# Kernel optimization log

Hardware: AMD Instinct MI355X
Metric: run time of the kernel (lower is better)

## Reference

```python
import jax, jax.numpy as jnp
import numpy as np

HIDDEN = 32
DN = ('NCHW', 'OIHW', 'NCHW')


def setup_inputs() -> dict:
    key = jax.random.key(0)
    ks = jax.random.split(key, 16)
    B = 32768
    s = lambda *sh: 1.0 / np.sqrt(np.prod(sh[1:]) if len(sh) > 1 else sh[0])
    inp = {
        'x': jax.random.normal(ks[0], (B, 12, 3, 4, 4), jnp.float32),
        'hour': jax.random.uniform(ks[1], (B, 1), jnp.float32),
        # ConvLSTM cell: Conv2d(3+32 -> 4*32, k=3, pad=1)
        'conv_w': jax.random.normal(ks[2], (4 * HIDDEN, 3 + HIDDEN, 3, 3), jnp.float32) * 0.05,
        'conv_b': jnp.zeros((4 * HIDDEN,), jnp.float32),
        # hour embedding: Linear(1,16) -> ReLU -> Linear(16,32)
        'he_w1': jax.random.normal(ks[3], (1, 16), jnp.float32),
        'he_b1': jnp.zeros((16,), jnp.float32),
        'he_w2': jax.random.normal(ks[4], (16, 32), jnp.float32) * 0.25,
        'he_b2': jnp.zeros((32,), jnp.float32),
        # decoder: Linear(544,256) -> ReLU -> Linear(256,128) -> ReLU -> Linear(128,30) -> Sigmoid
        'd_w1': jax.random.normal(ks[5], (32 * 4 * 4 + 32, 256), jnp.float32) * 0.04,
        'd_b1': jnp.zeros((256,), jnp.float32),
        'd_w2': jax.random.normal(ks[6], (256, 128), jnp.float32) * 0.06,
        'd_b2': jnp.zeros((128,), jnp.float32),
        'd_w3': jax.random.normal(ks[7], (128, 30), jnp.float32) * 0.09,
        'd_b3': jnp.zeros((30,), jnp.float32),
    }
    return inp


def _convlstm_scan(x, conv_w, conv_b):
    B, T, C, H, W = x.shape
    h0 = jnp.zeros((B, HIDDEN, H, W), x.dtype)
    c0 = jnp.zeros((B, HIDDEN, H, W), x.dtype)

    def step(carry, xt):
        h, c = carry
        inp = jnp.concatenate([xt, h], axis=1)  # [B, 3+32, 4, 4]
        gates = jax.lax.conv_general_dilated(
            inp, conv_w, (1, 1), 'SAME', dimension_numbers=DN)
        gates = gates + conv_b[None, :, None, None]
        i, f, o, g = jnp.split(gates, 4, axis=1)
        c_next = jax.nn.sigmoid(f) * c + jax.nn.sigmoid(i) * jnp.tanh(g)
        h_next = jax.nn.sigmoid(o) * jnp.tanh(c_next)
        return (h_next, c_next), None

    xs = jnp.swapaxes(x, 0, 1)  # [T, B, C, H, W]
    (h, c), _ = jax.lax.scan(step, (h0, c0), xs)
    return h


def reference(x, hour, conv_w, conv_b, he_w1, he_b1, he_w2, he_b2,
              d_w1, d_b1, d_w2, d_b2, d_w3, d_b3):
    B = x.shape[0]
    h = _convlstm_scan(x, conv_w, conv_b)            # [B, 32, 4, 4]
    spatial = h.reshape(B, -1)                        # [B, 512]
    hf = jax.nn.relu(hour @ he_w1 + he_b1) @ he_w2 + he_b2  # [B, 32]
    z = jnp.concatenate([spatial, hf], axis=1)        # [B, 544]
    z = jax.nn.relu(z @ d_w1 + d_b1)
    z = jax.nn.relu(z @ d_w2 + d_b2)                  # (dropout is identity in eval)
    out = jax.nn.sigmoid(z @ d_w3 + d_b3)
    return out.reshape(B, 10, 3)
```

## Files before the change

kernel.cpp:

```cpp
#include <hip/hip_runtime.h>

typedef _Float16 f16;
typedef _Float16 f16x4 __attribute__((ext_vector_type(4)));
typedef _Float16 f16x8 __attribute__((ext_vector_type(8)));
typedef float f32x2 __attribute__((ext_vector_type(2)));
typedef float f32x4 __attribute__((ext_vector_type(4)));

#define MFMA16(a, b, c) __builtin_amdgcn_mfma_f32_16x16x32_f16((a), (b), (c), 0, 0, 0)

__device__ __forceinline__ float rcp_(float x) { return __builtin_amdgcn_rcpf(x); }
__device__ __forceinline__ float sigm(float v) { return rcp_(1.0f + __expf(-v)); }
__device__ __forceinline__ float tanh_(float v) { return 1.0f - 2.0f * rcp_(__expf(2.0f * v) + 1.0f); }

#define XP 10368
#define WSO 11520
#define SMEMA 29952
#define NGRP 8192
#define GRID_REC 512

extern "C" __global__ __launch_bounds__(256, 2)
void hwq_rec(const float* __restrict__ gx, const float* __restrict__ ghour,
             const float* __restrict__ gcw, const float* __restrict__ gcb,
             const float* __restrict__ ghw1, const float* __restrict__ ghb1,
             const float* __restrict__ ghw2, const float* __restrict__ ghb2,
             f16* __restrict__ wz)
{
  __shared__ __align__(16) char smem[SMEMA];
  const int tid = threadIdx.x;
  const int lane = tid & 63;
  const int wv = tid >> 6;
  const int mg = wv & 1;
  const int ng = wv >> 1;
  const int lr = lane & 15;
  const int lk = lane >> 4;
  const int TOFF[9] = {0, 1, 2, 6, 7, 8, 12, 13, 14};
  const int pp0 = (lr >> 2) * 6 + (lr & 3);

  {
    float* za = (float*)smem;
    for (int i = tid; i < 2880; i += 256) za[i] = 0.0f;
    f16* axs = (f16*)(smem + WSO);
    for (int i = tid; i < 4096; i += 256) {
      int m = i >> 5, k = i & 31;
      int tau = k >> 2, sl = k & 3;
      int oc = ((m & 3) << 5) + (m >> 2);
      f16 v = (f16)0.0f;
      if (sl < 3) v = (f16)gcw[oc * 315 + sl * 9 + tau];
      else if (tau == 4) v = (f16)gcb[oc];
      axs[i] = v;
    }
    __syncthreads();
  }
  f16x8 Ax1[4], Ax2[4];
  {
    if (tid < 64) {
      int b = tid >> 4, p = tid & 15;
      int cell = ((p >> 2) + 1) * 6 + (p & 3) + 1;
      *(f16*)(smem + XP + b * 288 + cell * 8 + 6) = (f16)1.0f;
    }
    #pragma unroll
    for (int mt = 0; mt < 4; ++mt) {
      Ax1[mt] = *(const f16x8*)(smem + WSO + (mg * 64 + mt * 16 + lr) * 64 + lk * 16);
      int m = mg * 64 + mt * 16 + lr;
      int oc = ((m & 3) << 5) + (m >> 2);
      f16x8 f = {(f16)0, (f16)0, (f16)0, (f16)0, (f16)0, (f16)0, (f16)0, (f16)0};
      if (lk == 0) {
        f[0] = (f16)gcw[oc * 315 + 8];
        f[1] = (f16)gcw[oc * 315 + 17];
        f[2] = (f16)gcw[oc * 315 + 26];
      }
      Ax2[mt] = f;
    }
    __syncthreads();
  }
  f16x8 Ah[9][4];
  {
    f16* wst = (f16*)(smem + WSO);
    #pragma unroll
    for (int c = 0; c < 4; ++c) {
      for (int i = tid; i < 9216; i += 256) {
        int mrow = i / 288, rem = i - mrow * 288;
        int m = c * 32 + mrow;
        int oc = ((m & 3) << 5) + (m >> 2);
        wst[i] = (f16)gcw[oc * 315 + 27 + rem];
      }
      __syncthreads();
      if (mg == (c >> 1)) {
        #pragma unroll
        for (int mtl = 0; mtl < 2; ++mtl) {
          int mt = (c & 1) * 2 + mtl;
          #pragma unroll
          for (int tap = 0; tap < 9; ++tap) {
            f16x8 f;
            #pragma unroll
            for (int j = 0; j < 8; ++j)
              f[j] = wst[(mtl * 16 + lr) * 288 + (lk * 8 + j) * 9 + tap];
            Ah[tap][mt] = f;
          }
        }
      }
      __syncthreads();
    }
  }

  const int hb  = (ng * 2) * 2592 + pp0 * 72 + lk * 16;
  const int xpb = XP + (ng * 2) * 288 + pp0 * 8;
  const int wb  = (ng * 2) * 2592 + (pp0 + 7) * 72 + (mg * 16 + lk) * 2;
  const int xo0 = TOFF[2 * lk] * 8;
  const int xo1 = TOFF[2 * lk + 1] * 8;
  const bool stg = tid < 192;
  const int sb = tid / 48, srem = tid - sb * 48;
  const int sp = srem & 15, sic = srem >> 4;
  const int xdst = XP + sb * 288 + (((sp >> 2) + 1) * 6 + (sp & 3) + 1) * 8 + sic * 2;
  const int zb_ = tid >> 6, zc16 = (tid >> 2) & 15, zpart = tid & 3;
  const int zaddr = zb_ * 2592 + ((zc16 >> 2) * 6 + (zc16 & 3) + 7) * 72 + zpart * 16;

  for (int grp = blockIdx.x; grp < NGRP; grp += GRID_REC) {
    const int bg = grp << 2;
    const float* gxb = gx + (size_t)bg * 576;
    const float* xsrc = gxb + (size_t)sb * 576 + srem;

    {
      f32x2 z2 = {0.f, 0.f};
      *(f32x2*)(smem + zaddr) = z2;
      *(f32x2*)(smem + zaddr + 8) = z2;
    }
    if (stg) *(f16*)(smem + xdst) = (f16)xsrc[0];
    float cst[4][2];
    #pragma unroll
    for (int mt = 0; mt < 4; ++mt) { cst[mt][0] = 0.0f; cst[mt][1] = 0.0f; }
    __syncthreads();

    for (int t = 0; t < 12; ++t) {
      float xv = 0.0f;
      if (t < 11 && stg) xv = xsrc[(t + 1) * 48];

      f32x4 acc[4][2];
      #pragma unroll
      for (int mt = 0; mt < 4; ++mt)
        #pragma unroll
        for (int nt = 0; nt < 2; ++nt) { f32x4 z = {0.f, 0.f, 0.f, 0.f}; acc[mt][nt] = z; }

      #pragma unroll
      for (int tap = 0; tap < 9; ++tap) {
        const int to = TOFF[tap] * 72;
        #pragma unroll
        for (int nt = 0; nt < 2; ++nt) {
          f16x8 bf = *(const f16x8*)(smem + hb + nt * 2592 + to);
          #pragma unroll
          for (int mt = 0; mt < 4; ++mt)
            acc[mt][nt] = MFMA16(Ah[tap][mt], bf, acc[mt][nt]);
        }
      }
      #pragma unroll
      for (int nt = 0; nt < 2; ++nt) {
        const int base = xpb + nt * 288;
        f16x4 lo = *(const f16x4*)(smem + base + xo0);
        f16x4 hi = *(const f16x4*)(smem + base + xo1);
        f16x8 bf1 = __builtin_shufflevector(lo, hi, 0, 1, 2, 3, 4, 5, 6, 7);
        f16x4 l8 = *(const f16x4*)(smem + base + 112);
        f16x8 bf2 = __builtin_shufflevector(l8, l8, 0, 1, 2, 3, 0, 1, 2, 3);
        #pragma unroll
        for (int mt = 0; mt < 4; ++mt) {
          acc[mt][nt] = MFMA16(Ax1[mt], bf1, acc[mt][nt]);
          acc[mt][nt] = MFMA16(Ax2[mt], bf2, acc[mt][nt]);
        }
      }
      __syncthreads();

      #pragma unroll
      for (int mt = 0; mt < 4; ++mt) {
        #pragma unroll
        for (int nt = 0; nt < 2; ++nt) {
          float ig = sigm(acc[mt][nt][0]);
          float fg = sigm(acc[mt][nt][1]);
          float og = sigm(acc[mt][nt][2]);
          float gg = tanh_(acc[mt][nt][3]);
          float cn = fg * cst[mt][nt] + ig * gg;
          cst[mt][nt] = cn;
          f16 h = (f16)(og * tanh_(cn));
          if (t < 11) {
            *(f16*)(smem + wb + nt * 2592 + mt * 8) = h;
          } else {
            int ch = mg * 16 + mt * 4 + lk;
            wz[(size_t)(bg + ng * 2 + nt) * 544 + ch * 16 + lr] = h;
          }
        }
      }
      if (t < 11) {
        if (stg) *(f16*)(smem + xdst) = (f16)xv;
      } else if (tid < 128) {
        int b = tid >> 5, k2 = tid & 31;
        float h0 = ghour[bg + b];
        float a = ghb2[k2];
        #pragma unroll
        for (int ii = 0; ii < 16; ++ii) {
          float u = fmaxf(h0 * ghw1[ii] + ghb1[ii], 0.0f);
          a += u * ghw2[ii * 32 + k2];
        }
        wz[(size_t)(bg + b) * 544 + 512 + k2] = (f16)a;
      }
      __syncthreads();
    }
  }
}

extern "C" __global__ void hwq_prep(const float* __restrict__ gdw1,
                                    const float* __restrict__ gdw2,
                                    const float* __restrict__ gdw3,
                                    f16* __restrict__ w1t, f16* __restrict__ w2t,
                                    f16* __restrict__ w3t)
{
  int i0 = blockIdx.x * 256 + threadIdx.x;
  int stride = gridDim.x * 256;
  for (int idx = i0; idx < 139264; idx += stride) {
    int n = idx / 544, k = idx - n * 544;
    w1t[idx] = (f16)gdw1[k * 256 + n];
  }
  for (int idx = i0; idx < 32768; idx += stride) {
    int n = idx >> 8, k = idx & 255;
    w2t[idx] = (f16)gdw2[k * 128 + n];
  }
  for (int idx = i0; idx < 4096; idx += stride) {
    int n = idx >> 7, k = idx & 127;
    w3t[idx] = (n < 30) ? (f16)gdw3[k * 30 + n] : (f16)0.0f;
  }
}

extern "C" __global__ __launch_bounds__(256, 2)
void hwq_dec(const f16* __restrict__ wz, const f16* __restrict__ w1t,
             const f16* __restrict__ w2t, const f16* __restrict__ w3t,
             const float* __restrict__ gdb1, const float* __restrict__ gdb2,
             const float* __restrict__ gdb3, float* __restrict__ gout)
{
  __shared__ __align__(16) char smem[55296];
  f16* a1 = (f16*)smem;
  f16* a2 = (f16*)(smem + 35840);
  const int tid = threadIdx.x;
  const int lane = tid & 63;
  const int wv = tid >> 6;
  const int lr = lane & 15;
  const int lk = lane >> 4;
  const int s0 = blockIdx.x << 6;

  f32x4 acc1[4][4];
  #pragma unroll
  for (int nt = 0; nt < 4; ++nt) {
    float bb = gdb1[wv * 64 + nt * 16 + lr];
    f32x4 bv = {bb, bb, bb, bb};
    #pragma unroll
    for (int mt = 0; mt < 4; ++mt) acc1[mt][nt] = bv;
  }
  for (int kt = 0; kt < 17; ++kt) {
    f16x8 af[4];
    #pragma unroll
    for (int mt = 0; mt < 4; ++mt)
      af[mt] = *(const f16x8*)(wz + (size_t)(s0 + mt * 16 + lr) * 544 + kt * 32 + lk * 8);
    #pragma unroll
    for (int nt = 0; nt < 4; ++nt) {
      f16x8 bf = *(const f16x8*)(w1t + (size_t)(wv * 64 + nt * 16 + lr) * 544 + kt * 32 + lk * 8);
      #pragma unroll
      for (int mt = 0; mt < 4; ++mt)
        acc1[mt][nt] = MFMA16(af[mt], bf, acc1[mt][nt]);
    }
  }
  #pragma unroll
  for (int mt = 0; mt < 4; ++mt)
    #pragma unroll
    for (int nt = 0; nt < 4; ++nt) {
      int n = wv * 64 + nt * 16 + lr;
      #pragma unroll
      for (int r = 0; r < 4; ++r)
        a1[(mt * 16 + lk * 4 + r) * 280 + n] = (f16)fmaxf(acc1[mt][nt][r], 0.0f);
    }
  __syncthreads();

  f32x4 acc2[4][2];
  #pragma unroll
  for (int nt = 0; nt < 2; ++nt) {
    float bb = gdb2[wv * 32 + nt * 16 + lr];
    f32x4 bv = {bb, bb, bb, bb};
    #pragma unroll
    for (int mt = 0; mt < 4; ++mt) acc2[mt][nt] = bv;
  }
  for (int kt = 0; kt < 8; ++kt) {
    f16x8 af[4];
    #pragma unroll
    for (int mt = 0; mt < 4; ++mt)
      af[mt] = *(const f16x8*)(a1 + (mt * 16 + lr) * 280 + kt * 32 + lk * 8);
    #pragma unroll
    for (int nt = 0; nt < 2; ++nt) {
      f16x8 bf = *(const f16x8*)(w2t + (size_t)(wv * 32 + nt * 16 + lr) * 256 + kt * 32 + lk * 8);
      #pragma unroll
      for (int mt = 0; mt < 4; ++mt)
        acc2[mt][nt] = MFMA16(af[mt], bf, acc2[mt][nt]);
    }
  }
  __syncthreads();
  #pragma unroll
  for (int mt = 0; mt < 4; ++mt)
    #pragma unroll
    for (int nt = 0; nt < 2; ++nt) {
      int n = wv * 32 + nt * 16 + lr;
      #pragma unroll
      for (int r = 0; r < 4; ++r)
        a2[(mt * 16 + lk * 4 + r) * 152 + n] = (f16)fmaxf(acc2[mt][nt][r], 0.0f);
    }
  __syncthreads();

  if (wv < 2) {
    int n = wv * 16 + lr;
    float bb = (n < 30) ? gdb3[n] : 0.0f;
    f32x4 acc3[4];
    #pragma unroll
    for (int mt = 0; mt < 4; ++mt) { f32x4 bv = {bb, bb, bb, bb}; acc3[mt] = bv; }
    #pragma unroll
    for (int kt = 0; kt < 4; ++kt) {
      f16x8 bf = *(const f16x8*)(w3t + n * 128 + kt * 32 + lk * 8);
      #pragma unroll
      for (int mt = 0; mt < 4; ++mt) {
        f16x8 af = *(const f16x8*)(a2 + (mt * 16 + lr) * 152 + kt * 32 + lk * 8);
        acc3[mt] = MFMA16(af, bf, acc3[mt]);
      }
    }
    if (n < 30) {
      #pragma unroll
      for (int mt = 0; mt < 4; ++mt)
        #pragma unroll
        for (int r = 0; r < 4; ++r)
          gout[(size_t)(s0 + mt * 16 + lk * 4 + r) * 30 + n] = sigm(acc3[mt][r]);
    }
  }
}

typedef _Float16 f16x4m __attribute__((ext_vector_type(4)));
#define OFF_B 46080
#define SMEM_BYTES (46080 + 17408)

extern "C" __global__ __launch_bounds__(256, 1)
void hwq_fused_mono(const float* __restrict__ gx, const float* __restrict__ ghour,
               const float* __restrict__ gcw, const float* __restrict__ gcb,
               const float* __restrict__ ghw1, const float* __restrict__ ghb1,
               const float* __restrict__ ghw2, const float* __restrict__ ghb2,
               const float* __restrict__ gdw1, const float* __restrict__ gdb1,
               const float* __restrict__ gdw2, const float* __restrict__ gdb2,
               const float* __restrict__ gdw3, const float* __restrict__ gdb3,
               float* __restrict__ gout)
{
  __shared__ __align__(16) char smem[SMEM_BYTES];
  const int tid = threadIdx.x;
  const int lane = tid & 63;
  const int wv = tid >> 6;
  const int mg = wv & 1;
  const int ng = wv >> 1;
  const int lr = lane & 15;
  const int lk = lane >> 4;
  const int bg = blockIdx.x << 4;

  f16x8 Ah[9][4];
  {
    f16* wst = (f16*)(smem);
    #pragma unroll
    for (int c = 0; c < 2; ++c) {
      __syncthreads();
      for (int i = tid; i < 18432; i += 256) {
        int oc = i / 288, rem = i - oc * 288;
        wst[i] = (f16)gcw[(c * 64 + oc) * 315 + 27 + rem];
      }
      __syncthreads();
      #pragma unroll
      for (int g = 0; g < 2; ++g) {
        int ocl = g * 32 + mg * 16 + lr;
        #pragma unroll
        for (int tap = 0; tap < 9; ++tap) {
          f16x8 f;
          #pragma unroll
          for (int j = 0; j < 8; ++j)
            f[j] = wst[ocl * 288 + (lk * 8 + j) * 9 + tap];
          Ah[tap][c * 2 + g] = f;
        }
      }
    }
  }
  f16x8 Ax[4];
  {
    f16* xw = (f16*)(smem + OFF_B);
    __syncthreads();
    for (int i = tid; i < 3456; i += 256) {
      int oc = i / 27, rem = i - oc * 27;
      xw[i] = (f16)gcw[oc * 315 + rem];
    }
    __syncthreads();
    #pragma unroll
    for (int mt = 0; mt < 4; ++mt) {
      int oc = mt * 32 + mg * 16 + lr;
      f16x8 f;
      #pragma unroll
      for (int j = 0; j < 8; ++j) {
        int k = lk * 8 + j;
        int tap = (k * 11) >> 5;
        int ic = k - 3 * tap;
        f16 v = (f16)0.0f;
        if (k < 27) v = xw[oc * 27 + ic * 9 + tap];
        f[j] = v;
      }
      Ax[mt] = f;
    }
    __syncthreads();
  }

  float bias[4][4];
  #pragma unroll
  for (int mt = 0; mt < 4; ++mt)
    #pragma unroll
    for (int r = 0; r < 4; ++r)
      bias[mt][r] = gcb[mt * 32 + mg * 16 + lk * 4 + r];

  {
    float* za = (float*)smem;
    for (int i = tid; i < 11520; i += 256) za[i] = 0.0f;
    float* zb = (float*)(smem + OFF_B);
    for (int i = tid; i < 1152; i += 256) zb[i] = 0.0f;
    __syncthreads();
    for (int i = tid; i < 768; i += 256) {
      int b = i / 48, rem = i - b * 48;
      int pos = rem & 15;
      int ic = rem >> 4;
      int pp = (pos >> 2) * 6 + (pos & 3) + 7;
      *(f16*)(smem + OFF_B + b * 288 + pp * 8 + ic * 2) =
          (f16)gx[(size_t)(bg + b) * 576 + rem];
    }
    __syncthreads();
  }

  int hbase[8], xbase[8], wbase[8];
  #pragma unroll
  for (int nt = 0; nt < 8; ++nt) {
    int n = ng * 128 + nt * 16 + lr;
    int b = n >> 4, pos = n & 15;
    int pp0 = (pos >> 2) * 6 + (pos & 3);
    hbase[nt] = b * 2880 + pp0 * 80 + lk * 16;
    xbase[nt] = OFF_B + b * 288 + pp0 * 8;
    wbase[nt] = b * 2880 + (pp0 + 7) * 80 + (mg * 16 + lk * 4) * 2;
  }
  int xoff[8], xval[8];
  #pragma unroll
  for (int j = 0; j < 8; ++j) {
    int k = lk * 8 + j;
    int tap = (k * 11) >> 5;
    int ic = k - 3 * tap;
    xoff[j] = ((tap / 3) * 6 + (tap % 3)) * 8 + ic * 2;
    xval[j] = (k < 27);
  }

  const int TOFF[9] = {0, 1, 2, 6, 7, 8, 12, 13, 14};

  f32x4 cst[8];
  #pragma unroll
  for (int nt = 0; nt < 8; ++nt) { f32x4 z = {0.f, 0.f, 0.f, 0.f}; cst[nt] = z; }

  for (int t = 0; t < 12; ++t) {
    f32x4 acc[4][8];
    #pragma unroll
    for (int mt = 0; mt < 4; ++mt) {
      f32x4 bi = {bias[mt][0], bias[mt][1], bias[mt][2], bias[mt][3]};
      #pragma unroll
      for (int nt = 0; nt < 8; ++nt) acc[mt][nt] = bi;
    }
    #pragma unroll
    for (int tap = 0; tap < 9; ++tap) {
      #pragma unroll
      for (int nt = 0; nt < 8; ++nt) {
        f16x8 bf = *(const f16x8*)(smem + hbase[nt] + TOFF[tap] * 80);
        #pragma unroll
        for (int mt = 0; mt < 4; ++mt)
          acc[mt][nt] = MFMA16(Ah[tap][mt], bf, acc[mt][nt]);
      }
    }
    #pragma unroll
    for (int nt = 0; nt < 8; ++nt) {
      f16x8 bf;
      #pragma unroll
      for (int j = 0; j < 8; ++j) {
        int a = xval[j] ? (xbase[nt] + xoff[j]) : OFF_B;
        bf[j] = *(const f16*)(smem + a);
      }
      #pragma unroll
      for (int mt = 0; mt < 4; ++mt)
        acc[mt][nt] = MFMA16(Ax[mt], bf, acc[mt][nt]);
    }
    __syncthreads();

    #pragma unroll
    for (int nt = 0; nt < 8; ++nt) {
      f16 hh[4];
      #pragma unroll
      for (int r = 0; r < 4; ++r) {
        float ig = sigm(acc[0][nt][r]);
        float fg = sigm(acc[1][nt][r]);
        float og = sigm(acc[2][nt][r]);
        float gg = tanh_(acc[3][nt][r]);
        float cn = fg * cst[nt][r] + ig * gg;
        cst[nt][r] = cn;
        hh[r] = (f16)(og * tanh_(cn));
      }
      if (t < 11) {
        f16x4m hv = {hh[0], hh[1], hh[2], hh[3]};
        *(f16x4m*)(smem + wbase[nt]) = hv;
      } else {
        int n = ng * 128 + nt * 16 + lr;
        int b = n >> 4, pos = n & 15;
        int ch0 = mg * 16 + lk * 4;
        #pragma unroll
        for (int r = 0; r < 4; ++r)
          *(f16*)(smem + OFF_B + b * 1088 + (ch0 + r) * 32 + pos * 2) = hh[r];
      }
    }
    if (t < 11) {
      for (int i = tid; i < 768; i += 256) {
        int b = i / 48, rem = i - b * 48;
        int pos = rem & 15;
        int ic = rem >> 4;
        int pp = (pos >> 2) * 6 + (pos & 3) + 7;
        *(f16*)(smem + OFF_B + b * 288 + pp * 8 + ic * 2) =
            (f16)gx[(size_t)(bg + b) * 576 + (t + 1) * 48 + rem];
      }
    } else {
      for (int i = tid; i < 512; i += 256) {
        int b = i >> 5, k2 = i & 31;
        float h0 = ghour[bg + b];
        float a = ghb2[k2];
        #pragma unroll
        for (int ii = 0; ii < 16; ++ii) {
          float u = fmaxf(h0 * ghw1[ii] + ghb1[ii], 0.0f);
          a += u * ghw2[ii * 32 + k2];
        }
        *(f16*)(smem + OFF_B + b * 1088 + (512 + k2) * 2) = (f16)a;
      }
    }
    __syncthreads();
  }

  f16* zz  = (f16*)(smem + OFF_B);
  f16* wch = (f16*)(smem);
  f16* a1  = (f16*)(smem + 16384);
  f16* a2  = (f16*)(smem + 24576);
  f16* w3s = (f16*)(smem + 28672);

  f32x4 acc1[4];
  #pragma unroll
  for (int i = 0; i < 4; ++i) { f32x4 z = {0.f, 0.f, 0.f, 0.f}; acc1[i] = z; }
  for (int kt = 0; kt < 17; ++kt) {
    __syncthreads();
    for (int i = tid; i < 8192; i += 256) {
      int k = i >> 8, n = i & 255;
      wch[i] = (f16)gdw1[(kt * 32 + k) * 256 + n];
    }
    __syncthreads();
    f16x8 af = *(const f16x8*)((char*)zz + lr * 1088 + (kt * 32 + lk * 8) * 2);
    #pragma unroll
    for (int nt = 0; nt < 4; ++nt) {
      int n = (wv * 4 + nt) * 16 + lr;
      f16x8 bf;
      #pragma unroll
      for (int j = 0; j < 8; ++j) bf[j] = wch[(lk * 8 + j) * 256 + n];
      acc1[nt] = MFMA16(af, bf, acc1[nt]);
    }
  }
  __syncthreads();
  #pragma unroll
  for (int nt = 0; nt < 4; ++nt) {
    int n = (wv * 4 + nt) * 16 + lr;
    float bb = gdb1[n];
    #pragma unroll
    for (int r = 0; r < 4; ++r)
      a1[(lk * 4 + r) * 256 + n] = (f16)fmaxf(acc1[nt][r] + bb, 0.0f);
  }

  f32x4 acc2[2];
  #pragma unroll
  for (int i = 0; i < 2; ++i) { f32x4 z = {0.f, 0.f, 0.f, 0.f}; acc2[i] = z; }
  for (int kt = 0; kt < 8; ++kt) {
    __syncthreads();
    for (int i = tid; i < 4096; i += 256) {
      int k = i >> 7, n = i & 127;
      wch[i] = (f16)gdw2[(kt * 32 + k) * 128 + n];
    }
    __syncthreads();
    f16x8 af = *(const f16x8*)((char*)a1 + lr * 512 + (kt * 32 + lk * 8) * 2);
    #pragma unroll
    for (int nt = 0; nt < 2; ++nt) {
      int n = (wv * 2 + nt) * 16 + lr;
      f16x8 bf;
      #pragma unroll
      for (int j = 0; j < 8; ++j) bf[j] = wch[(lk * 8 + j) * 128 + n];
      acc2[nt] = MFMA16(af, bf, acc2[nt]);
    }
  }
  __syncthreads();
  #pragma unroll
  for (int nt = 0; nt < 2; ++nt) {
    int n = (wv * 2 + nt) * 16 + lr;
    float bb = gdb2[n];
    #pragma unroll
    for (int r = 0; r < 4; ++r)
      a2[(lk * 4 + r) * 128 + n] = (f16)fmaxf(acc2[nt][r] + bb, 0.0f);
  }
  __syncthreads();

  for (int i = tid; i < 4096; i += 256) {
    int k = i >> 5, n = i & 31;
    w3s[i] = (n < 30) ? (f16)gdw3[k * 30 + n] : (f16)0.0f;
  }
  __syncthreads();
  if (wv < 2) {
    f32x4 acc3 = {0.f, 0.f, 0.f, 0.f};
    int n = wv * 16 + lr;
    #pragma unroll
    for (int kt = 0; kt < 4; ++kt) {
      f16x8 af = *(const f16x8*)((char*)a2 + lr * 256 + (kt * 32 + lk * 8) * 2);
      f16x8 bf;
      #pragma unroll
      for (int j = 0; j < 8; ++j) bf[j] = w3s[(kt * 32 + lk * 8 + j) * 32 + n];
      acc3 = MFMA16(af, bf, acc3);
    }
    if (n < 30) {
      float bb = gdb3[n];
      #pragma unroll
      for (int r = 0; r < 4; ++r) {
        float v = sigm(acc3[r] + bb);
        gout[(size_t)(bg + lk * 4 + r) * 30 + n] = v;
      }
    }
  }
}

extern "C" void kernel_launch(void* const* d_in, const int* in_sizes, int n_in,
                              void* d_out, int out_size, void* d_ws, size_t ws_size,
                              hipStream_t stream) {
  (void)in_sizes; (void)n_in; (void)out_size;
  const size_t W1OFF = 35651584;
  const size_t W2OFF = W1OFF + 278528;
  const size_t W3OFF = W2OFF + 65536;
  const size_t NEED  = W3OFF + 8192;
  if (ws_size >= NEED) {
    f16* wzp = (f16*)d_ws;
    f16* w1t = (f16*)((char*)d_ws + W1OFF);
    f16* w2t = (f16*)((char*)d_ws + W2OFF);
    f16* w3t = (f16*)((char*)d_ws + W3OFF);
    hwq_prep<<<256, 256, 0, stream>>>((const float*)d_in[8], (const float*)d_in[10],
                                      (const float*)d_in[12], w1t, w2t, w3t);
    hwq_rec<<<GRID_REC, 256, 0, stream>>>(
        (const float*)d_in[0], (const float*)d_in[1], (const float*)d_in[2],
        (const float*)d_in[3], (const float*)d_in[4], (const float*)d_in[5],
        (const float*)d_in[6], (const float*)d_in[7], wzp);
    hwq_dec<<<512, 256, 0, stream>>>(wzp, w1t, w2t, w3t,
                                     (const float*)d_in[9], (const float*)d_in[11],
                                     (const float*)d_in[13], (float*)d_out);
  } else {
    hwq_fused_mono<<<2048, 256, 0, stream>>>(
        (const float*)d_in[0],  (const float*)d_in[1],  (const float*)d_in[2],
        (const float*)d_in[3],  (const float*)d_in[4],  (const float*)d_in[5],
        (const float*)d_in[6],  (const float*)d_in[7],  (const float*)d_in[8],
        (const float*)d_in[9],  (const float*)d_in[10], (const float*)d_in[11],
        (const float*)d_in[12], (const float*)d_in[13], (float*)d_out);
  }
}
```

Measured before the change: 716.4 us.

## Double-buffer hidden state and input in LDS to drop a barrier per step

```diff
diff --git a/kernel.cpp b/kernel.cpp
--- a/kernel.cpp
+++ b/kernel.cpp
@@ -3,7 +3,6 @@
 typedef _Float16 f16;
 typedef _Float16 f16x4 __attribute__((ext_vector_type(4)));
 typedef _Float16 f16x8 __attribute__((ext_vector_type(8)));
-typedef float f32x2 __attribute__((ext_vector_type(2)));
 typedef float f32x4 __attribute__((ext_vector_type(4)));
 
 #define MFMA16(a, b, c) __builtin_amdgcn_mfma_f32_16x16x32_f16((a), (b), (c), 0, 0, 0)
@@ -12,9 +11,9 @@
 __device__ __forceinline__ float sigm(float v) { return rcp_(1.0f + __expf(-v)); }
 __device__ __forceinline__ float tanh_(float v) { return 1.0f - 2.0f * rcp_(__expf(2.0f * v) + 1.0f); }
 
-#define XP 10368
-#define WSO 11520
-#define SMEMA 29952
+#define XP 18432
+#define WSO 20736
+#define SMEMA 39168
 #define NGRP 8192
 #define GRID_REC 512
 
@@ -38,7 +37,7 @@
 
   {
     float* za = (float*)smem;
-    for (int i = tid; i < 2880; i += 256) za[i] = 0.0f;
+    for (int i = tid; i < 5184; i += 256) za[i] = 0.0f;
     f16* axs = (f16*)(smem + WSO);
     for (int i = tid; i < 4096; i += 256) {
       int m = i >> 5, k = i & 31;
@@ -53,10 +52,10 @@
   }
   f16x8 Ax1[4], Ax2[4];
   {
-    if (tid < 64) {
-      int b = tid >> 4, p = tid & 15;
+    if (tid < 128) {
+      int buf = tid >> 6, b = (tid >> 4) & 3, p = tid & 15;
       int cell = ((p >> 2) + 1) * 6 + (p & 3) + 1;
-      *(f16*)(smem + XP + b * 288 + cell * 8 + 6) = (f16)1.0f;
+      *(f16*)(smem + XP + buf * 1152 + b * 288 + cell * 8 + 6) = (f16)1.0f;
     }
     #pragma unroll
     for (int mt = 0; mt < 4; ++mt) {
@@ -103,17 +102,17 @@
     }
   }
 
-  const int hb  = (ng * 2) * 2592 + pp0 * 72 + lk * 16;
-  const int xpb = XP + (ng * 2) * 288 + pp0 * 8;
-  const int wb  = (ng * 2) * 2592 + (pp0 + 7) * 72 + (mg * 16 + lk) * 2;
+  const int hb  = (ng * 2) * 2304 + lk * 576 + pp0 * 16;
+  const int xpb = (ng * 2) * 288 + pp0 * 8;
+  const int wbase = (ng * 2) * 2304 + (mg * 2) * 576 + (pp0 + 7) * 16 + lk * 2;
   const int xo0 = TOFF[2 * lk] * 8;
   const int xo1 = TOFF[2 * lk + 1] * 8;
   const bool stg = tid < 192;
   const int sb = tid / 48, srem = tid - sb * 48;
   const int sp = srem & 15, sic = srem >> 4;
   const int xdst = XP + sb * 288 + (((sp >> 2) + 1) * 6 + (sp & 3) + 1) * 8 + sic * 2;
-  const int zb_ = tid >> 6, zc16 = (tid >> 2) & 15, zpart = tid & 3;
-  const int zaddr = zb_ * 2592 + ((zc16 >> 2) * 6 + (zc16 & 3) + 7) * 72 + zpart * 16;
+  const int zb_ = tid >> 6, zkg = (tid >> 4) & 3, zc = tid & 15;
+  const int zaddr = zb_ * 2304 + zkg * 576 + (((zc >> 2) + 1) * 6 + (zc & 3) + 1) * 16;
 
   for (int grp = blockIdx.x; grp < NGRP; grp += GRID_REC) {
     const int bg = grp << 2;
@@ -121,9 +120,8 @@
     const float* xsrc = gxb + (size_t)sb * 576 + srem;
 
     {
-      f32x2 z2 = {0.f, 0.f};
-      *(f32x2*)(smem + zaddr) = z2;
-      *(f32x2*)(smem + zaddr + 8) = z2;
+      f32x4 z4 = {0.f, 0.f, 0.f, 0.f};
+      *(f32x4*)(smem + zaddr) = z4;
     }
     if (stg) *(f16*)(smem + xdst) = (f16)xsrc[0];
     float cst[4][2];
@@ -131,77 +129,85 @@
     for (int mt = 0; mt < 4; ++mt) { cst[mt][0] = 0.0f; cst[mt][1] = 0.0f; }
     __syncthreads();
 
-    for (int t = 0; t < 12; ++t) {
-      float xv = 0.0f;
-      if (t < 11 && stg) xv = xsrc[(t + 1) * 48];
-
-      f32x4 acc[4][2];
-      #pragma unroll
-      for (int mt = 0; mt < 4; ++mt)
-        #pragma unroll
-        for (int nt = 0; nt < 2; ++nt) { f32x4 z = {0.f, 0.f, 0.f, 0.f}; acc[mt][nt] = z; }
-
-      #pragma unroll
-      for (int tap = 0; tap < 9; ++tap) {
-        const int to = TOFF[tap] * 72;
-        #pragma unroll
-        for (int nt = 0; nt < 2; ++nt) {
-          f16x8 bf = *(const f16x8*)(smem + hb + nt * 2592 + to);
-          #pragma unroll
-          for (int mt = 0; mt < 4; ++mt)
-            acc[mt][nt] = MFMA16(Ah[tap][mt], bf, acc[mt][nt]);
-        }
-      }
-      #pragma unroll
-      for (int nt = 0; nt < 2; ++nt) {
-        const int base = xpb + nt * 288;
-        f16x4 lo = *(const f16x4*)(smem + base + xo0);
-        f16x4 hi = *(const f16x4*)(smem + base + xo1);
-        f16x8 bf1 = __builtin_shufflevector(lo, hi, 0, 1, 2, 3, 4, 5, 6, 7);
-        f16x4 l8 = *(const f16x4*)(smem + base + 112);
-        f16x8 bf2 = __builtin_shufflevector(l8, l8, 0, 1, 2, 3, 0, 1, 2, 3);
-        #pragma unroll
-        for (int mt = 0; mt < 4; ++mt) {
-          acc[mt][nt] = MFMA16(Ax1[mt], bf1, acc[mt][nt]);
-          acc[mt][nt] = MFMA16(Ax2[mt], bf2, acc[mt][nt]);
-        }
-      }
-      __syncthreads();
-
-      #pragma unroll
-      for (int mt = 0; mt < 4; ++mt) {
-        #pragma unroll
-        for (int nt = 0; nt < 2; ++nt) {
-          float ig = sigm(acc[mt][nt][0]);
-          float fg = sigm(acc[mt][nt][1]);
-          float og = sigm(acc[mt][nt][2]);
-          float gg = tanh_(acc[mt][nt][3]);
-          float cn = fg * cst[mt][nt] + ig * gg;
-          cst[mt][nt] = cn;
-          f16 h = (f16)(og * tanh_(cn));
-          if (t < 11) {
-            *(f16*)(smem + wb + nt * 2592 + mt * 8) = h;
-          } else {
-            int ch = mg * 16 + mt * 4 + lk;
-            wz[(size_t)(bg + ng * 2 + nt) * 544 + ch * 16 + lr] = h;
-          }
-        }
-      }
-      if (t < 11) {
-        if (stg) *(f16*)(smem + xdst) = (f16)xv;
-      } else if (tid < 128) {
-        int b = tid >> 5, k2 = tid & 31;
-        float h0 = ghour[bg + b];
-        float a = ghb2[k2];
-        #pragma unroll
-        for (int ii = 0; ii < 16; ++ii) {
-          float u = fmaxf(h0 * ghw1[ii] + ghb1[ii], 0.0f);
-          a += u * ghw2[ii * 32 + k2];
-        }
-        wz[(size_t)(bg + b) * 544 + 512 + k2] = (f16)a;
-      }
-      __syncthreads();
-    }
+#define STEP(T, RB)                                                              \
+    {                                                                            \
+      const int t = (T);                                                         \
+      float xv = 0.0f;                                                           \
+      if (t < 11 && stg) xv = xsrc[(t + 1) * 48];                                \
+      f32x4 acc[4][2];                                                           \
+      _Pragma("unroll")                                                          \
+      for (int mt = 0; mt < 4; ++mt) {                                           \
+        f32x4 z = {0.f, 0.f, 0.f, 0.f};                                          \
+        acc[mt][0] = z; acc[mt][1] = z;                                          \
+      }                                                                          \
+      const char* hB = smem + (RB) * 9216 + hb;                                  \
+      _Pragma("unroll")                                                          \
+      for (int tap = 0; tap < 9; ++tap) {                                        \
+        const int to = TOFF[tap] * 16;                                           \
+        _Pragma("unroll")                                                        \
+        for (int nt = 0; nt < 2; ++nt) {                                         \
+          f16x8 bf = *(const f16x8*)(hB + nt * 2304 + to);                       \
+          _Pragma("unroll")                                                      \
+          for (int mt = 0; mt < 4; ++mt)                                         \
+            acc[mt][nt] = MFMA16(Ah[tap][mt], bf, acc[mt][nt]);                  \
+        }                                                                        \
+      }                                                                          \
+      const char* xB = smem + XP + (RB) * 1152 + xpb;                            \
+      _Pragma("unroll")                                                          \
+      for (int nt = 0; nt < 2; ++nt) {                                           \
+        const char* base = xB + nt * 288;                                        \
+        f16x4 lo = *(const f16x4*)(base + xo0);                                  \
+        f16x4 hi = *(const f16x4*)(base + xo1);                                  \
+        f16x8 bf1 = __builtin_shufflevector(lo, hi, 0, 1, 2, 3, 4, 5, 6, 7);     \
+        f16x4 l8 = *(const f16x4*)(base + 112);                                  \
+        f16x8 bf2 = __builtin_shufflevector(l8, l8, 0, 1, 2, 3, 0, 1, 2, 3);     \
+        _Pragma("unroll")                                                        \
+        for (int mt = 0; mt < 4; ++mt) {                                         \
+          acc[mt][nt] = MFMA16(Ax1[mt], bf1, acc[mt][nt]);                       \
+          acc[mt][nt] = MFMA16(Ax2[mt], bf2, acc[mt][nt]);                       \
+        }                                                                        \
+      }                                                                          \
+      char* hW = smem + (1 - (RB)) * 9216 + wbase;                               \
+      _Pragma("unroll")                                                          \
+      for (int mt = 0; mt < 4; ++mt) {                                           \
+        _Pragma("unroll")                                                        \
+        for (int nt = 0; nt < 2; ++nt) {                                         \
+          float ig = sigm(acc[mt][nt][0]);                                       \
+          float fg = sigm(acc[mt][nt][1]);                                       \
+          float og = sigm(acc[mt][nt][2]);                                       \
+          float gg = tanh_(acc[mt][nt][3]);                                      \
+          float cn = fg * cst[mt][nt] + ig * gg;                                 \
+          cst[mt][nt] = cn;                                                      \
+          f16 h = (f16)(og * tanh_(cn));                                         \
+          if (t < 11) {                                                          \
+            *(f16*)(hW + nt * 2304 + (mt >> 1) * 576 + (mt & 1) * 8) = h;        \
+          } else {                                                               \
+            int ch = mg * 16 + mt * 4 + lk;                                      \
+            wz[(size_t)(bg + ng * 2 + nt) * 544 + ch * 16 + lr] = h;             \
+          }                                                                      \
+        }                                                                        \
+      }                                                                          \
+      if (t < 11) {                                                              \
+        if (stg) *(f16*)(smem + (1 - (RB)) * 1152 + xdst) = (f16)xv;             \
+      } else if (tid < 128) {                                                    \
+        int b = tid >> 5, k2 = tid & 31;                                         \
+        float h0 = ghour[bg + b];                                                \
+        float a = ghb2[k2];                                                      \
+        _Pragma("unroll")                                                        \
+        for (int ii = 0; ii < 16; ++ii) {                                        \
+          float u = fmaxf(h0 * ghw1[ii] + ghb1[ii], 0.0f);                       \
+          a += u * ghw2[ii * 32 + k2];                                           \
+        }                                                                        \
+        wz[(size_t)(bg + b) * 544 + 512 + k2] = (f16)a;                          \
+      }                                                                          \
+      __syncthreads();                                                           \
+    }
+
+    for (int tb = 0; tb < 12; tb += 2) {
+      STEP(tb, 0)
+      STEP(tb + 1, 1)
+    }
+#undef STEP
   }
 }
 
```

Measured after the change: 1.002 ms. 1.4x slower.
